# Kernel tuning notes

Measured on AMD Instinct MI355X. Metric: run time of the kernel, lower is better.

The kernel has to match this reference:

```python
import jax, jax.numpy as jnp
import numpy as np

# GeoFormer.generate_proposal constants (cfg.threshold_ins, cfg.min_pts_num,
# instance classes start at semantic id 4 on ScanNet)
THRESHOLD = 0.5
MIN_PTS_NUM = 50
MIN_INST_CLASS = 4


def setup_inputs() -> dict:
    key = jax.random.key(0)
    k1, k2, k3, k4 = jax.random.split(key, 4)
    B, Q, N, C = 4, 128, 50000, 20
    mask_logits = jax.random.normal(k1, (B, Q, N), dtype=jnp.float32)
    cls_logits = jax.random.normal(k2, (B, Q, C), dtype=jnp.float32)
    seg_pred = jax.random.randint(k3, (B, N), 0, C, dtype=jnp.int64)
    fg_idxs = jax.random.randint(k4, (B * N,), 0, 300000, dtype=jnp.int64)
    return {"mask_logits": mask_logits, "cls_logits": cls_logits,
            "seg_pred": seg_pred, "fg_idxs": fg_idxs}


def reference(mask_logits, cls_logits, seg_pred, fg_idxs):
    # mask_logits: [B, Q, N]  per-query point-mask logits (dense form of the
    #   per-batch list in the original; batch_offsets become the B dim)
    # cls_logits:  [B, Q, C]  per-query class logits
    # seg_pred:    [B, N]     per-point semantic prediction
    # fg_idxs:     [B*N]      foreground -> original point id map
    B, Q, N = mask_logits.shape
    m = jax.nn.sigmoid(mask_logits)                         # [B, Q, N]
    cls_pred = jnp.argmax(cls_logits, axis=2)               # [B, Q]

    # (mask_logit_b[n] > threshold) & (seg_pred == cls_logits_pred[b, n])
    sel = (m > THRESHOLD) & (seg_pred[:, None, :] == cls_pred[:, :, None])  # [B,Q,N]
    cnt = sel.sum(axis=-1)                                  # [B, Q] proposal sizes

    # score = mean of sigmoid over selected points
    msel = jnp.where(sel, m, jnp.zeros((), m.dtype))
    scores = msel.sum(axis=-1) / jnp.maximum(cnt, 1).astype(m.dtype)  # [B, Q]

    # skip if too few points or a background/wall class (< 4)
    valid = (cnt >= MIN_PTS_NUM) & (cls_pred >= MIN_INST_CLASS)       # [B, Q]

    proposal_masks = sel & valid[:, :, None]                # dense proposal_idx
    scores = jnp.where(valid, scores, jnp.zeros((), scores.dtype))
    global_ids = fg_idxs.reshape(B, N)                      # fg_idxs remap per point
    return proposal_masks, scores, valid, cls_pred, global_ids
```

## Files before the change

kernel.cpp:

```cpp
#include <hip/hip_runtime.h>
#include <math.h>

#define BB 4
#define QQ 128
#define NN 50000
#define CC 20
#define ROWS (BB * QQ)
#define NV4 (NN / 4)
#define TPB 256
#define UNROLL 4
#define BPR 13
#define THRESH_CNT 50
#define MIN_CLS 4

typedef float f32x4 __attribute__((ext_vector_type(4)));
typedef int   i32x4 __attribute__((ext_vector_type(4)));

struct Ws {
    float sum[ROWS];
    int   cnt[ROWS];
    int   cls[ROWS];
    int   valid[ROWS];
};

__global__ void k0_argmax_zero(const float* __restrict__ cls_logits, Ws* ws) {
    int r = blockIdx.x * blockDim.x + threadIdx.x;
    if (r >= ROWS) return;
    const float* p = cls_logits + r * CC;
    float best = p[0];
    int bi = 0;
    #pragma unroll
    for (int c = 1; c < CC; ++c) {
        float v = p[c];
        if (v > best) { best = v; bi = c; }
    }
    ws->cls[r] = bi;
    ws->sum[r] = 0.0f;
    ws->cnt[r] = 0;
}

__global__ __launch_bounds__(256) void k1_select(
        const float* __restrict__ mask_logits,
        const int*   __restrict__ seg_pred,
        float* __restrict__ out_mask,
        Ws* __restrict__ ws) {
    const int row = blockIdx.y;
    const int b   = row >> 7;
    const int cls = ws->cls[row];

    const f32x4* __restrict__ ml = (const f32x4*)(mask_logits + (size_t)row * NN);
    const i32x4* __restrict__ sp = (const i32x4*)(seg_pred + b * NN);
    f32x4* __restrict__ om = (f32x4*)(out_mask + (size_t)row * NN);

    const int idx0 = blockIdx.x * (TPB * UNROLL) + threadIdx.x;

    f32x4 v[UNROLL];
    i32x4 s[UNROLL];
    bool  act[UNROLL];
    #pragma unroll
    for (int j = 0; j < UNROLL; ++j) {
        int idx = idx0 + j * TPB;
        act[j] = (idx < NV4);
        if (act[j]) {
            v[j] = ml[idx];
            s[j] = sp[idx];
        }
    }

    float lsum = 0.0f;
    int   lcnt = 0;
    #pragma unroll
    for (int j = 0; j < UNROLL; ++j) {
        if (!act[j]) continue;
        int idx = idx0 + j * TPB;
        f32x4 vv = v[j];
        i32x4 ss = s[j];
        bool s0 = (vv.x > 0.0f) & (ss.x == cls);
        bool s1 = (vv.y > 0.0f) & (ss.y == cls);
        bool s2 = (vv.z > 0.0f) & (ss.z == cls);
        bool s3 = (vv.w > 0.0f) & (ss.w == cls);
        float g0 = 1.0f / (1.0f + __expf(-vv.x));
        float g1 = 1.0f / (1.0f + __expf(-vv.y));
        float g2 = 1.0f / (1.0f + __expf(-vv.z));
        float g3 = 1.0f / (1.0f + __expf(-vv.w));
        f32x4 o;
        o.x = s0 ? 1.0f : 0.0f;
        o.y = s1 ? 1.0f : 0.0f;
        o.z = s2 ? 1.0f : 0.0f;
        o.w = s3 ? 1.0f : 0.0f;
        lsum += (s0 ? g0 : 0.0f) + (s1 ? g1 : 0.0f)
              + (s2 ? g2 : 0.0f) + (s3 ? g3 : 0.0f);
        lcnt += (int)s0 + (int)s1 + (int)s2 + (int)s3;
        __builtin_nontemporal_store(o, &om[idx]);
    }

    #pragma unroll
    for (int off = 32; off > 0; off >>= 1) {
        lsum += __shfl_down(lsum, off);
        lcnt += __shfl_down(lcnt, off);
    }
    __shared__ float ssum[4];
    __shared__ int   scnt[4];
    const int wave = threadIdx.x >> 6;
    const int lane = threadIdx.x & 63;
    if (lane == 0) { ssum[wave] = lsum; scnt[wave] = lcnt; }
    __syncthreads();
    if (threadIdx.x == 0) {
        float ts = ssum[0] + ssum[1] + ssum[2] + ssum[3];
        int   tc = scnt[0] + scnt[1] + scnt[2] + scnt[3];
        atomicAdd(&ws->sum[row], ts);
        atomicAdd(&ws->cnt[row], tc);
    }
}

__global__ void k2_finalize_gids(const int* __restrict__ fg,
                                 float* __restrict__ out,
                                 Ws* __restrict__ ws) {
    const int idx = blockIdx.x * blockDim.x + threadIdx.x;
    if (idx < ROWS) {
        int   cnt = ws->cnt[idx];
        int   cls = ws->cls[idx];
        float sum = ws->sum[idx];
        int valid = (cnt >= THRESH_CNT) && (cls >= MIN_CLS);
        ws->valid[idx] = valid;
        float* tail = out + (size_t)ROWS * NN;
        tail[idx]            = valid ? (sum / (float)max(cnt, 1)) : 0.0f;
        tail[ROWS + idx]     = valid ? 1.0f : 0.0f;
        tail[2 * ROWS + idx] = (float)cls;
    }
    const int nv4 = (BB * NN) / 4;
    if (idx < nv4) {
        float* gids = out + (size_t)ROWS * NN + 3 * ROWS;
        i32x4 v = ((const i32x4*)fg)[idx];
        f32x4 o;
        o.x = (float)v.x; o.y = (float)v.y; o.z = (float)v.z; o.w = (float)v.w;
        __builtin_nontemporal_store(o, &((f32x4*)gids)[idx]);
    }
}

__global__ __launch_bounds__(256) void k3_fixup(
        float* __restrict__ out_mask, const Ws* __restrict__ ws) {
    const int row = blockIdx.y;
    if (ws->valid[row]) return;
    f32x4* __restrict__ om = (f32x4*)(out_mask + (size_t)row * NN);
    const f32x4 z = {0.0f, 0.0f, 0.0f, 0.0f};
    const int idx0 = blockIdx.x * (TPB * UNROLL) + threadIdx.x;
    #pragma unroll
    for (int j = 0; j < UNROLL; ++j) {
        int idx = idx0 + j * TPB;
        if (idx < NV4) __builtin_nontemporal_store(z, &om[idx]);
    }
}

extern "C" void kernel_launch(void* const* d_in, const int* in_sizes, int n_in,
                              void* d_out, int out_size, void* d_ws, size_t ws_size,
                              hipStream_t stream) {
    const float* mask_logits = (const float*)d_in[0];
    const float* cls_logits  = (const float*)d_in[1];
    const int*   seg_pred    = (const int*)d_in[2];
    const int*   fg_idxs     = (const int*)d_in[3];

    float* out = (float*)d_out;
    Ws* ws = (Ws*)d_ws;

    float* out_mask = out;

    k0_argmax_zero<<<(ROWS + 255) / 256, 256, 0, stream>>>(cls_logits, ws);

    dim3 g1(BPR, ROWS);
    k1_select<<<g1, TPB, 0, stream>>>(mask_logits, seg_pred, out_mask, ws);

    const int gids_blocks = ((BB * NN) / 4 + 255) / 256;
    k2_finalize_gids<<<gids_blocks, 256, 0, stream>>>(fg_idxs, out, ws);

    k3_fixup<<<g1, TPB, 0, stream>>>(out_mask, ws);
}
```

Measured before the change: 195.6 us.

## Pack selection bits in workspace, expand to the final mask after validity is known

The select kernel now writes a compact per-row bitmask to workspace instead of the full float mask. A separate expand kernel, run after finalize, writes the float mask with validity already applied. This removes the extra zeroing pass over invalid rows and makes the first pass read-only on the large output. The cost is an extra kernel launch plus a small bitmask round-trip, and it needs enough workspace. If workspace is too small, a fused fallback keeps the old three-pass scheme.

```diff
diff --git a/kernel.cpp b/kernel.cpp
--- a/kernel.cpp
+++ b/kernel.cpp
@@ -10,6 +10,7 @@
 #define TPB 256
 #define UNROLL 4
 #define BPR 13
+#define WPR 1568
 #define THRESH_CNT 50
 #define MIN_CLS 4
 
@@ -39,59 +40,62 @@
     ws->cnt[r] = 0;
 }
 
-__global__ __launch_bounds__(256) void k1_select(
+
+__global__ __launch_bounds__(256) void k1_pack(
         const float* __restrict__ mask_logits,
         const int*   __restrict__ seg_pred,
-        float* __restrict__ out_mask,
+        unsigned int* __restrict__ bits,
         Ws* __restrict__ ws) {
     const int row = blockIdx.y;
     const int b   = row >> 7;
     const int cls = ws->cls[row];
 
-    const f32x4* __restrict__ ml = (const f32x4*)(mask_logits + (size_t)row * NN);
-    const i32x4* __restrict__ sp = (const i32x4*)(seg_pred + b * NN);
-    f32x4* __restrict__ om = (f32x4*)(out_mask + (size_t)row * NN);
-
-    const int idx0 = blockIdx.x * (TPB * UNROLL) + threadIdx.x;
+    const f32x4* __restrict__ ml = (const f32x4*)mask_logits + (size_t)row * NV4;
+    const i32x4* __restrict__ sp = (const i32x4*)seg_pred + b * NV4;
+
+    const int base = blockIdx.x * (TPB * UNROLL) + threadIdx.x * UNROLL;
 
     f32x4 v[UNROLL];
     i32x4 s[UNROLL];
     bool  act[UNROLL];
     #pragma unroll
     for (int j = 0; j < UNROLL; ++j) {
-        int idx = idx0 + j * TPB;
-        act[j] = (idx < NV4);
+        act[j] = (base + j) < NV4;
         if (act[j]) {
-            v[j] = ml[idx];
-            s[j] = sp[idx];
+            v[j] = ml[base + j];
+            s[j] = sp[base + j];
         }
     }
 
+    unsigned int b16 = 0;
     float lsum = 0.0f;
     int   lcnt = 0;
     #pragma unroll
     for (int j = 0; j < UNROLL; ++j) {
-        if (!act[j]) continue;
-        int idx = idx0 + j * TPB;
-        f32x4 vv = v[j];
-        i32x4 ss = s[j];
-        bool s0 = (vv.x > 0.0f) & (ss.x == cls);
-        bool s1 = (vv.y > 0.0f) & (ss.y == cls);
-        bool s2 = (vv.z > 0.0f) & (ss.z == cls);
-        bool s3 = (vv.w > 0.0f) & (ss.w == cls);
-        float g0 = 1.0f / (1.0f + __expf(-vv.x));
-        float g1 = 1.0f / (1.0f + __expf(-vv.y));
-        float g2 = 1.0f / (1.0f + __expf(-vv.z));
-        float g3 = 1.0f / (1.0f + __expf(-vv.w));
-        f32x4 o;
-        o.x = s0 ? 1.0f : 0.0f;
-        o.y = s1 ? 1.0f : 0.0f;
-        o.z = s2 ? 1.0f : 0.0f;
-        o.w = s3 ? 1.0f : 0.0f;
-        lsum += (s0 ? g0 : 0.0f) + (s1 ? g1 : 0.0f)
-              + (s2 ? g2 : 0.0f) + (s3 ? g3 : 0.0f);
-        lcnt += (int)s0 + (int)s1 + (int)s2 + (int)s3;
-        __builtin_nontemporal_store(o, &om[idx]);
+        if (act[j]) {
+            f32x4 vv = v[j];
+            i32x4 ss = s[j];
+            unsigned s0 = (vv.x > 0.0f) & (ss.x == cls);
+            unsigned s1 = (vv.y > 0.0f) & (ss.y == cls);
+            unsigned s2 = (vv.z > 0.0f) & (ss.z == cls);
+            unsigned s3 = (vv.w > 0.0f) & (ss.w == cls);
+            b16 |= (s0 | (s1 << 1) | (s2 << 2) | (s3 << 3)) << (4 * j);
+            float g0 = 1.0f / (1.0f + __expf(-vv.x));
+            float g1 = 1.0f / (1.0f + __expf(-vv.y));
+            float g2 = 1.0f / (1.0f + __expf(-vv.z));
+            float g3 = 1.0f / (1.0f + __expf(-vv.w));
+            lsum += (s0 ? g0 : 0.0f) + (s1 ? g1 : 0.0f)
+                  + (s2 ? g2 : 0.0f) + (s3 ? g3 : 0.0f);
+            lcnt += (int)(s0 + s1 + s2 + s3);
+        }
+    }
+
+    unsigned int partner = __shfl_xor((int)b16, 1);
+    if ((threadIdx.x & 1) == 0) {
+        unsigned int word = b16 | (partner << 16);
+        const int h = blockIdx.x * TPB + threadIdx.x;
+        const int w = h >> 1;
+        if (w < WPR) bits[(size_t)row * WPR + w] = word;
     }
 
     #pragma unroll
@@ -110,6 +114,31 @@
         int   tc = scnt[0] + scnt[1] + scnt[2] + scnt[3];
         atomicAdd(&ws->sum[row], ts);
         atomicAdd(&ws->cnt[row], tc);
+    }
+}
+
+__global__ __launch_bounds__(256) void k_expand(
+        const unsigned int* __restrict__ bits,
+        const Ws* __restrict__ ws,
+        float* __restrict__ out_mask) {
+    const int row = blockIdx.y;
+    const float on = ws->valid[row] ? 1.0f : 0.0f;
+    const unsigned int* __restrict__ wb = bits + (size_t)row * WPR;
+    f32x4* __restrict__ om = (f32x4*)out_mask + (size_t)row * NV4;
+    const int idx0 = blockIdx.x * (TPB * UNROLL) + threadIdx.x;
+    #pragma unroll
+    for (int j = 0; j < UNROLL; ++j) {
+        int idx = idx0 + j * TPB;
+        if (idx < NV4) {
+            unsigned int word = wb[idx >> 3];
+            unsigned int nib = word >> ((idx & 7) * 4);
+            f32x4 o;
+            o.x = (nib & 1u) ? on : 0.0f;
+            o.y = (nib & 2u) ? on : 0.0f;
+            o.z = (nib & 4u) ? on : 0.0f;
+            o.w = (nib & 8u) ? on : 0.0f;
+            __builtin_nontemporal_store(o, &om[idx]);
+        }
     }
 }
 
@@ -138,6 +167,60 @@
     }
 }
 
+
+__global__ __launch_bounds__(256) void k1_select_fused(
+        const float* __restrict__ mask_logits,
+        const int*   __restrict__ seg_pred,
+        float* __restrict__ out_mask,
+        Ws* __restrict__ ws) {
+    const int row = blockIdx.y;
+    const int b   = row >> 7;
+    const int cls = ws->cls[row];
+    const f32x4* __restrict__ ml = (const f32x4*)(mask_logits + (size_t)row * NN);
+    const i32x4* __restrict__ sp = (const i32x4*)(seg_pred + b * NN);
+    f32x4* __restrict__ om = (f32x4*)(out_mask + (size_t)row * NN);
+    const int idx0 = blockIdx.x * (TPB * UNROLL) + threadIdx.x;
+    float lsum = 0.0f;
+    int   lcnt = 0;
+    #pragma unroll
+    for (int j = 0; j < UNROLL; ++j) {
+        int idx = idx0 + j * TPB;
+        if (idx >= NV4) continue;
+        f32x4 vv = ml[idx];
+        i32x4 ss = sp[idx];
+        bool s0 = (vv.x > 0.0f) & (ss.x == cls);
+        bool s1 = (vv.y > 0.0f) & (ss.y == cls);
+        bool s2 = (vv.z > 0.0f) & (ss.z == cls);
+        bool s3 = (vv.w > 0.0f) & (ss.w == cls);
+        f32x4 o;
+        o.x = s0 ? 1.0f : 0.0f;
+        o.y = s1 ? 1.0f : 0.0f;
+        o.z = s2 ? 1.0f : 0.0f;
+        o.w = s3 ? 1.0f : 0.0f;
+        lsum += (s0 ? 1.0f / (1.0f + __expf(-vv.x)) : 0.0f)
+              + (s1 ? 1.0f / (1.0f + __expf(-vv.y)) : 0.0f)
+              + (s2 ? 1.0f / (1.0f + __expf(-vv.z)) : 0.0f)
+              + (s3 ? 1.0f / (1.0f + __expf(-vv.w)) : 0.0f);
+        lcnt += (int)s0 + (int)s1 + (int)s2 + (int)s3;
+        __builtin_nontemporal_store(o, &om[idx]);
+    }
+    #pragma unroll
+    for (int off = 32; off > 0; off >>= 1) {
+        lsum += __shfl_down(lsum, off);
+        lcnt += __shfl_down(lcnt, off);
+    }
+    __shared__ float ssum[4];
+    __shared__ int   scnt[4];
+    const int wave = threadIdx.x >> 6;
+    const int lane = threadIdx.x & 63;
+    if (lane == 0) { ssum[wave] = lsum; scnt[wave] = lcnt; }
+    __syncthreads();
+    if (threadIdx.x == 0) {
+        atomicAdd(&ws->sum[row], ssum[0] + ssum[1] + ssum[2] + ssum[3]);
+        atomicAdd(&ws->cnt[row], scnt[0] + scnt[1] + scnt[2] + scnt[3]);
+    }
+}
+
 __global__ __launch_bounds__(256) void k3_fixup(
         float* __restrict__ out_mask, const Ws* __restrict__ ws) {
     const int row = blockIdx.y;
@@ -162,16 +245,25 @@
 
     float* out = (float*)d_out;
     Ws* ws = (Ws*)d_ws;
+    unsigned int* bits = (unsigned int*)((char*)d_ws + sizeof(Ws));
 
     float* out_mask = out;
 
+    const size_t ws_needed = sizeof(Ws) + (size_t)ROWS * WPR * sizeof(unsigned int);
+    const bool use_split = (ws_size >= ws_needed);
+
     k0_argmax_zero<<<(ROWS + 255) / 256, 256, 0, stream>>>(cls_logits, ws);
 
     dim3 g1(BPR, ROWS);
-    k1_select<<<g1, TPB, 0, stream>>>(mask_logits, seg_pred, out_mask, ws);
-
     const int gids_blocks = ((BB * NN) / 4 + 255) / 256;
-    k2_finalize_gids<<<gids_blocks, 256, 0, stream>>>(fg_idxs, out, ws);
-
-    k3_fixup<<<g1, TPB, 0, stream>>>(out_mask, ws);
-}
+
+    if (use_split) {
+        k1_pack<<<g1, TPB, 0, stream>>>(mask_logits, seg_pred, bits, ws);
+        k2_finalize_gids<<<gids_blocks, 256, 0, stream>>>(fg_idxs, out, ws);
+        k_expand<<<g1, TPB, 0, stream>>>(bits, ws, out_mask);
+    } else {
+        k1_select_fused<<<g1, TPB, 0, stream>>>(mask_logits, seg_pred, out_mask, ws);
+        k2_finalize_gids<<<gids_blocks, 256, 0, stream>>>(fg_idxs, out, ws);
+        k3_fixup<<<g1, TPB, 0, stream>>>(out_mask, ws);
+    }
+}
```

After: 206.4 us. 1.06x slower.

## Fuse select, finalize and fixup into one row-per-block kernel with class bitmasks

Applied to the files above, without the earlier changes.

Replaces the four-kernel pipeline with one block per (batch, query) row. Each block computes the argmax itself, reduces count and sum locally, decides validity, and writes the mask only once with the validity already applied. This removes the atomics, the workspace round trip, and the second pass that rewrote invalid rows with zeros. A pre-pass packs seg_pred into per-class bitmasks, so each row reads one bit per point instead of an int. The cost is that only 512 blocks of 512 threads run, each holding its selection bits in registers, which may lower parallelism.

```diff
diff --git a/kernel.cpp b/kernel.cpp
--- a/kernel.cpp
+++ b/kernel.cpp
@@ -7,91 +7,93 @@
 #define CC 20
 #define ROWS (BB * QQ)
 #define NV4 (NN / 4)
+#define W32 1568
 #define TPB 256
-#define UNROLL 4
-#define BPR 13
+#define TPB2 512
+#define ITER 25
 #define THRESH_CNT 50
 #define MIN_CLS 4
 
 typedef float f32x4 __attribute__((ext_vector_type(4)));
 typedef int   i32x4 __attribute__((ext_vector_type(4)));
 
-struct Ws {
-    float sum[ROWS];
-    int   cnt[ROWS];
-    int   cls[ROWS];
-    int   valid[ROWS];
-};
-
-__global__ void k0_argmax_zero(const float* __restrict__ cls_logits, Ws* ws) {
-    int r = blockIdx.x * blockDim.x + threadIdx.x;
-    if (r >= ROWS) return;
-    const float* p = cls_logits + r * CC;
-    float best = p[0];
-    int bi = 0;
+__global__ void k_pre_classbit(const int* __restrict__ seg,
+                               unsigned int* __restrict__ classbit) {
+    const int b = blockIdx.y;
+    const int p = blockIdx.x * TPB + threadIdx.x;
+    const int lane = threadIdx.x & 63;
+    const int cl = (p < NN) ? seg[b * NN + p] : -1;
+    const int w0 = (blockIdx.x * TPB + (threadIdx.x & ~63)) >> 5;
     #pragma unroll
-    for (int c = 1; c < CC; ++c) {
-        float v = p[c];
-        if (v > best) { best = v; bi = c; }
+    for (int c = 0; c < CC; ++c) {
+        unsigned long long m = __ballot(cl == c);
+        if (lane == 0)
+            classbit[((size_t)b * CC + c) * W32 + w0]     = (unsigned int)m;
+        if (lane == 32)
+            classbit[((size_t)b * CC + c) * W32 + w0 + 1] = (unsigned int)(m >> 32);
     }
-    ws->cls[r] = bi;
-    ws->sum[r] = 0.0f;
-    ws->cnt[r] = 0;
 }
 
-__global__ __launch_bounds__(256) void k1_select(
+template <bool USE_BITS>
+__global__ __launch_bounds__(TPB2) void k_fused(
         const float* __restrict__ mask_logits,
+        const float* __restrict__ cls_logits,
         const int*   __restrict__ seg_pred,
-        float* __restrict__ out_mask,
-        Ws* __restrict__ ws) {
-    const int row = blockIdx.y;
+        const unsigned int* __restrict__ classbit,
+        float* __restrict__ out) {
+    const int row = blockIdx.x;
     const int b   = row >> 7;
-    const int cls = ws->cls[row];
+    const int tid = threadIdx.x;
 
-    const f32x4* __restrict__ ml = (const f32x4*)(mask_logits + (size_t)row * NN);
-    const i32x4* __restrict__ sp = (const i32x4*)(seg_pred + b * NN);
-    f32x4* __restrict__ om = (f32x4*)(out_mask + (size_t)row * NN);
+    __shared__ float s_logit[CC];
+    __shared__ int   s_cls;
+    __shared__ float s_on;
+    if (tid < CC) s_logit[tid] = cls_logits[row * CC + tid];
+    __syncthreads();
+    if (tid == 0) {
+        float best = s_logit[0];
+        int bi = 0;
+        #pragma unroll
+        for (int c = 1; c < CC; ++c) {
+            if (s_logit[c] > best) { best = s_logit[c]; bi = c; }
+        }
+        s_cls = bi;
+    }
+    __syncthreads();
+    const int cls = s_cls;
 
-    const int idx0 = blockIdx.x * (TPB * UNROLL) + threadIdx.x;
+    const f32x4* __restrict__ ml = (const f32x4*)mask_logits + (size_t)row * NV4;
+    const unsigned int* __restrict__ cb =
+        classbit + ((size_t)b * CC + cls) * W32;
+    const i32x4* __restrict__ sp = (const i32x4*)seg_pred + (size_t)b * NV4;
 
-    f32x4 v[UNROLL];
-    i32x4 s[UNROLL];
-    bool  act[UNROLL];
-    #pragma unroll
-    for (int j = 0; j < UNROLL; ++j) {
-        int idx = idx0 + j * TPB;
-        act[j] = (idx < NV4);
-        if (act[j]) {
-            v[j] = ml[idx];
-            s[j] = sp[idx];
-        }
-    }
-
+    unsigned int bw[4] = {0u, 0u, 0u, 0u};
     float lsum = 0.0f;
     int   lcnt = 0;
     #pragma unroll
-    for (int j = 0; j < UNROLL; ++j) {
-        if (!act[j]) continue;
-        int idx = idx0 + j * TPB;
-        f32x4 vv = v[j];
-        i32x4 ss = s[j];
-        bool s0 = (vv.x > 0.0f) & (ss.x == cls);
-        bool s1 = (vv.y > 0.0f) & (ss.y == cls);
-        bool s2 = (vv.z > 0.0f) & (ss.z == cls);
-        bool s3 = (vv.w > 0.0f) & (ss.w == cls);
-        float g0 = 1.0f / (1.0f + __expf(-vv.x));
-        float g1 = 1.0f / (1.0f + __expf(-vv.y));
-        float g2 = 1.0f / (1.0f + __expf(-vv.z));
-        float g3 = 1.0f / (1.0f + __expf(-vv.w));
-        f32x4 o;
-        o.x = s0 ? 1.0f : 0.0f;
-        o.y = s1 ? 1.0f : 0.0f;
-        o.z = s2 ? 1.0f : 0.0f;
-        o.w = s3 ? 1.0f : 0.0f;
-        lsum += (s0 ? g0 : 0.0f) + (s1 ? g1 : 0.0f)
-              + (s2 ? g2 : 0.0f) + (s3 ? g3 : 0.0f);
-        lcnt += (int)s0 + (int)s1 + (int)s2 + (int)s3;
-        __builtin_nontemporal_store(o, &om[idx]);
+    for (int it = 0; it < ITER; ++it) {
+        const int idx = it * TPB2 + tid;
+        if (idx < NV4) {
+            f32x4 vv = ml[idx];
+            unsigned int nib;
+            if (USE_BITS) {
+                unsigned int cw = cb[idx >> 3];
+                nib = (cw >> ((tid & 7) * 4)) & 0xFu;
+            } else {
+                i32x4 ss = sp[idx];
+                nib = ((ss.x == cls) ? 1u : 0u) | ((ss.y == cls) ? 2u : 0u)
+                    | ((ss.z == cls) ? 4u : 0u) | ((ss.w == cls) ? 8u : 0u);
+            }
+            unsigned int se = ((vv.x > 0.0f) ? 1u : 0u) | ((vv.y > 0.0f) ? 2u : 0u)
+                            | ((vv.z > 0.0f) ? 4u : 0u) | ((vv.w > 0.0f) ? 8u : 0u);
+            unsigned int sel = se & nib;
+            lsum += ((sel & 1u) ? 1.0f / (1.0f + __expf(-vv.x)) : 0.0f)
+                  + ((sel & 2u) ? 1.0f / (1.0f + __expf(-vv.y)) : 0.0f)
+                  + ((sel & 4u) ? 1.0f / (1.0f + __expf(-vv.z)) : 0.0f)
+                  + ((sel & 8u) ? 1.0f / (1.0f + __expf(-vv.w)) : 0.0f);
+            lcnt += __popc(sel);
+            bw[it >> 3] |= sel << (4 * (it & 7));
+        }
     }
 
     #pragma unroll
@@ -99,56 +101,51 @@
         lsum += __shfl_down(lsum, off);
         lcnt += __shfl_down(lcnt, off);
     }
-    __shared__ float ssum[4];
-    __shared__ int   scnt[4];
-    const int wave = threadIdx.x >> 6;
-    const int lane = threadIdx.x & 63;
+    __shared__ float ssum[TPB2 / 64];
+    __shared__ int   scnt[TPB2 / 64];
+    const int wave = tid >> 6;
+    const int lane = tid & 63;
     if (lane == 0) { ssum[wave] = lsum; scnt[wave] = lcnt; }
     __syncthreads();
-    if (threadIdx.x == 0) {
-        float ts = ssum[0] + ssum[1] + ssum[2] + ssum[3];
-        int   tc = scnt[0] + scnt[1] + scnt[2] + scnt[3];
-        atomicAdd(&ws->sum[row], ts);
-        atomicAdd(&ws->cnt[row], tc);
+    if (tid == 0) {
+        float ts = 0.0f;
+        int   tc = 0;
+        #pragma unroll
+        for (int w = 0; w < TPB2 / 64; ++w) { ts += ssum[w]; tc += scnt[w]; }
+        const int valid = (tc >= THRESH_CNT) && (cls >= MIN_CLS);
+        float* tail = out + (size_t)ROWS * NN;
+        tail[row]            = valid ? (ts / (float)(tc > 1 ? tc : 1)) : 0.0f;
+        tail[ROWS + row]     = valid ? 1.0f : 0.0f;
+        tail[2 * ROWS + row] = (float)cls;
+        s_on = valid ? 1.0f : 0.0f;
+    }
+    __syncthreads();
+    const float on = s_on;
+
+    f32x4* __restrict__ om = (f32x4*)out + (size_t)row * NV4;
+    #pragma unroll
+    for (int it = 0; it < ITER; ++it) {
+        const int idx = it * TPB2 + tid;
+        if (idx < NV4) {
+            const unsigned int nib = (bw[it >> 3] >> (4 * (it & 7))) & 0xFu;
+            f32x4 o;
+            o.x = (nib & 1u) ? on : 0.0f;
+            o.y = (nib & 2u) ? on : 0.0f;
+            o.z = (nib & 4u) ? on : 0.0f;
+            o.w = (nib & 8u) ? on : 0.0f;
+            __builtin_nontemporal_store(o, &om[idx]);
+        }
     }
 }
 
-__global__ void k2_finalize_gids(const int* __restrict__ fg,
-                                 float* __restrict__ out,
-                                 Ws* __restrict__ ws) {
+__global__ void k_gids(const int* __restrict__ fg, float* __restrict__ out) {
     const int idx = blockIdx.x * blockDim.x + threadIdx.x;
-    if (idx < ROWS) {
-        int   cnt = ws->cnt[idx];
-        int   cls = ws->cls[idx];
-        float sum = ws->sum[idx];
-        int valid = (cnt >= THRESH_CNT) && (cls >= MIN_CLS);
-        ws->valid[idx] = valid;
-        float* tail = out + (size_t)ROWS * NN;
-        tail[idx]            = valid ? (sum / (float)max(cnt, 1)) : 0.0f;
-        tail[ROWS + idx]     = valid ? 1.0f : 0.0f;
-        tail[2 * ROWS + idx] = (float)cls;
-    }
     const int nv4 = (BB * NN) / 4;
     if (idx < nv4) {
-        float* gids = out + (size_t)ROWS * NN + 3 * ROWS;
         i32x4 v = ((const i32x4*)fg)[idx];
         f32x4 o;
         o.x = (float)v.x; o.y = (float)v.y; o.z = (float)v.z; o.w = (float)v.w;
-        __builtin_nontemporal_store(o, &((f32x4*)gids)[idx]);
-    }
-}
-
-__global__ __launch_bounds__(256) void k3_fixup(
-        float* __restrict__ out_mask, const Ws* __restrict__ ws) {
-    const int row = blockIdx.y;
-    if (ws->valid[row]) return;
-    f32x4* __restrict__ om = (f32x4*)(out_mask + (size_t)row * NN);
-    const f32x4 z = {0.0f, 0.0f, 0.0f, 0.0f};
-    const int idx0 = blockIdx.x * (TPB * UNROLL) + threadIdx.x;
-    #pragma unroll
-    for (int j = 0; j < UNROLL; ++j) {
-        int idx = idx0 + j * TPB;
-        if (idx < NV4) __builtin_nontemporal_store(z, &om[idx]);
+        __builtin_nontemporal_store(o, &((f32x4*)out)[idx]);
     }
 }
 
@@ -161,17 +158,22 @@
     const int*   fg_idxs     = (const int*)d_in[3];
 
     float* out = (float*)d_out;
-    Ws* ws = (Ws*)d_ws;
+    unsigned int* classbit = (unsigned int*)d_ws;
 
-    float* out_mask = out;
+    float* out_gids = out + (size_t)ROWS * NN + 3 * ROWS;
 
-    k0_argmax_zero<<<(ROWS + 255) / 256, 256, 0, stream>>>(cls_logits, ws);
+    const size_t cb_bytes = (size_t)BB * CC * W32 * sizeof(unsigned int);
+    const bool use_bits = (ws_size >= cb_bytes);
 
-    dim3 g1(BPR, ROWS);
-    k1_select<<<g1, TPB, 0, stream>>>(mask_logits, seg_pred, out_mask, ws);
+    if (use_bits) {
+        dim3 gp((NN + TPB - 1) / TPB, BB);
+        k_pre_classbit<<<gp, TPB, 0, stream>>>(seg_pred, classbit);
+        k_fused<true><<<ROWS, TPB2, 0, stream>>>(
+            mask_logits, cls_logits, seg_pred, classbit, out);
+    } else {
+        k_fused<false><<<ROWS, TPB2, 0, stream>>>(
+            mask_logits, cls_logits, seg_pred, classbit, out);
+    }
 
-    const int gids_blocks = ((BB * NN) / 4 + 255) / 256;
-    k2_finalize_gids<<<gids_blocks, 256, 0, stream>>>(fg_idxs, out, ws);
-
-    k3_fixup<<<g1, TPB, 0, stream>>>(out_mask, ws);
+    k_gids<<<((BB * NN) / 4 + TPB - 1) / TPB, TPB, 0, stream>>>(fg_idxs, out_gids);
 }
```

Result: slower. 205.2 us (+4.9%).

## Precompute per-class bitmasks of seg_pred to shrink per-row segment loads

Applied to the files above, without the earlier changes.

Adds a pre-pass that packs seg_pred into one bitmask per (batch, class) using wave ballots and stores it in workspace. The main select kernel then reads one 32-bit word per 8 threads instead of a 16-byte int vector per thread, cutting seg_pred read traffic by about 32x. It adds an extra kernel launch and relies on workspace size, falling back to the old path if the workspace is too small. Sigmoid is also evaluated only on selected lanes via bit tests.

```diff
diff --git a/kernel.cpp b/kernel.cpp
--- a/kernel.cpp
+++ b/kernel.cpp
@@ -10,6 +10,7 @@
 #define TPB 256
 #define UNROLL 4
 #define BPR 13
+#define W32 1568
 #define THRESH_CNT 50
 #define MIN_CLS 4
 
@@ -39,31 +40,58 @@
     ws->cnt[r] = 0;
 }
 
-__global__ __launch_bounds__(256) void k1_select(
+__global__ void k_pre_classbit(const int* __restrict__ seg,
+                               unsigned int* __restrict__ classbit) {
+    const int b = blockIdx.y;
+    const int p = blockIdx.x * TPB + threadIdx.x;
+    const int lane = threadIdx.x & 63;
+    const int cl = (p < NN) ? seg[b * NN + p] : -1;
+    const int w0 = (blockIdx.x * TPB + (threadIdx.x & ~63)) >> 5;
+    #pragma unroll
+    for (int c = 0; c < CC; ++c) {
+        unsigned long long m = __ballot(cl == c);
+        if (lane == 0)
+            classbit[((size_t)b * CC + c) * W32 + w0]     = (unsigned int)m;
+        if (lane == 32)
+            classbit[((size_t)b * CC + c) * W32 + w0 + 1] = (unsigned int)(m >> 32);
+    }
+}
+
+template <bool USE_BITS>
+__global__ __launch_bounds__(256) void k1_main(
         const float* __restrict__ mask_logits,
         const int*   __restrict__ seg_pred,
+        const unsigned int* __restrict__ classbit,
         float* __restrict__ out_mask,
         Ws* __restrict__ ws) {
     const int row = blockIdx.y;
     const int b   = row >> 7;
     const int cls = ws->cls[row];
-
-    const f32x4* __restrict__ ml = (const f32x4*)(mask_logits + (size_t)row * NN);
-    const i32x4* __restrict__ sp = (const i32x4*)(seg_pred + b * NN);
-    f32x4* __restrict__ om = (f32x4*)(out_mask + (size_t)row * NN);
-
-    const int idx0 = blockIdx.x * (TPB * UNROLL) + threadIdx.x;
-
-    f32x4 v[UNROLL];
-    i32x4 s[UNROLL];
-    bool  act[UNROLL];
+    const int tid = threadIdx.x;
+
+    const f32x4* __restrict__ ml = (const f32x4*)mask_logits + (size_t)row * NV4;
+    const i32x4* __restrict__ sp = (const i32x4*)seg_pred + (size_t)b * NV4;
+    const unsigned int* __restrict__ cb = classbit + ((size_t)b * CC + cls) * W32;
+    f32x4* __restrict__ om = (f32x4*)out_mask + (size_t)row * NV4;
+
+    const f32x4 vz = {0.0f, 0.0f, 0.0f, 0.0f};
+
+    int          idx[UNROLL];
+    bool         act[UNROLL];
+    f32x4        v[UNROLL];
+    unsigned int nib[UNROLL];
     #pragma unroll
     for (int j = 0; j < UNROLL; ++j) {
-        int idx = idx0 + j * TPB;
-        act[j] = (idx < NV4);
-        if (act[j]) {
-            v[j] = ml[idx];
-            s[j] = sp[idx];
+        idx[j] = blockIdx.x * (TPB * UNROLL) + j * TPB + tid;
+        act[j] = idx[j] < NV4;
+        v[j] = act[j] ? ml[idx[j]] : vz;
+        if (USE_BITS) {
+            unsigned int cw = act[j] ? cb[idx[j] >> 3] : 0u;
+            nib[j] = (cw >> ((tid & 7) * 4)) & 0xFu;
+        } else {
+            i32x4 ss = act[j] ? sp[idx[j]] : i32x4{-1, -1, -1, -1};
+            nib[j] = ((ss.x == cls) ? 1u : 0u) | ((ss.y == cls) ? 2u : 0u)
+                   | ((ss.z == cls) ? 4u : 0u) | ((ss.w == cls) ? 8u : 0u);
         }
     }
 
@@ -71,27 +99,21 @@
     int   lcnt = 0;
     #pragma unroll
     for (int j = 0; j < UNROLL; ++j) {
-        if (!act[j]) continue;
-        int idx = idx0 + j * TPB;
         f32x4 vv = v[j];
-        i32x4 ss = s[j];
-        bool s0 = (vv.x > 0.0f) & (ss.x == cls);
-        bool s1 = (vv.y > 0.0f) & (ss.y == cls);
-        bool s2 = (vv.z > 0.0f) & (ss.z == cls);
-        bool s3 = (vv.w > 0.0f) & (ss.w == cls);
-        float g0 = 1.0f / (1.0f + __expf(-vv.x));
-        float g1 = 1.0f / (1.0f + __expf(-vv.y));
-        float g2 = 1.0f / (1.0f + __expf(-vv.z));
-        float g3 = 1.0f / (1.0f + __expf(-vv.w));
+        unsigned int se = ((vv.x > 0.0f) ? 1u : 0u) | ((vv.y > 0.0f) ? 2u : 0u)
+                        | ((vv.z > 0.0f) ? 4u : 0u) | ((vv.w > 0.0f) ? 8u : 0u);
+        unsigned int sel = se & nib[j];
+        lsum += ((sel & 1u) ? 1.0f / (1.0f + __expf(-vv.x)) : 0.0f)
+              + ((sel & 2u) ? 1.0f / (1.0f + __expf(-vv.y)) : 0.0f)
+              + ((sel & 4u) ? 1.0f / (1.0f + __expf(-vv.z)) : 0.0f)
+              + ((sel & 8u) ? 1.0f / (1.0f + __expf(-vv.w)) : 0.0f);
+        lcnt += __popc(sel);
         f32x4 o;
-        o.x = s0 ? 1.0f : 0.0f;
-        o.y = s1 ? 1.0f : 0.0f;
-        o.z = s2 ? 1.0f : 0.0f;
-        o.w = s3 ? 1.0f : 0.0f;
-        lsum += (s0 ? g0 : 0.0f) + (s1 ? g1 : 0.0f)
-              + (s2 ? g2 : 0.0f) + (s3 ? g3 : 0.0f);
-        lcnt += (int)s0 + (int)s1 + (int)s2 + (int)s3;
-        __builtin_nontemporal_store(o, &om[idx]);
+        o.x = (sel & 1u) ? 1.0f : 0.0f;
+        o.y = (sel & 2u) ? 1.0f : 0.0f;
+        o.z = (sel & 4u) ? 1.0f : 0.0f;
+        o.w = (sel & 8u) ? 1.0f : 0.0f;
+        if (act[j]) __builtin_nontemporal_store(o, &om[idx[j]]);
     }
 
     #pragma unroll
@@ -101,15 +123,13 @@
     }
     __shared__ float ssum[4];
     __shared__ int   scnt[4];
-    const int wave = threadIdx.x >> 6;
-    const int lane = threadIdx.x & 63;
+    const int wave = tid >> 6;
+    const int lane = tid & 63;
     if (lane == 0) { ssum[wave] = lsum; scnt[wave] = lcnt; }
     __syncthreads();
-    if (threadIdx.x == 0) {
-        float ts = ssum[0] + ssum[1] + ssum[2] + ssum[3];
-        int   tc = scnt[0] + scnt[1] + scnt[2] + scnt[3];
-        atomicAdd(&ws->sum[row], ts);
-        atomicAdd(&ws->cnt[row], tc);
+    if (tid == 0) {
+        atomicAdd(&ws->sum[row], ssum[0] + ssum[1] + ssum[2] + ssum[3]);
+        atomicAdd(&ws->cnt[row], scnt[0] + scnt[1] + scnt[2] + scnt[3]);
     }
 }
 
@@ -142,7 +162,7 @@
         float* __restrict__ out_mask, const Ws* __restrict__ ws) {
     const int row = blockIdx.y;
     if (ws->valid[row]) return;
-    f32x4* __restrict__ om = (f32x4*)(out_mask + (size_t)row * NN);
+    f32x4* __restrict__ om = (f32x4*)out_mask + (size_t)row * NV4;
     const f32x4 z = {0.0f, 0.0f, 0.0f, 0.0f};
     const int idx0 = blockIdx.x * (TPB * UNROLL) + threadIdx.x;
     #pragma unroll
@@ -162,16 +182,29 @@
 
     float* out = (float*)d_out;
     Ws* ws = (Ws*)d_ws;
+    unsigned int* classbit = (unsigned int*)((char*)d_ws + sizeof(Ws));
 
     float* out_mask = out;
 
+    const size_t ws_needed = sizeof(Ws)
+        + (size_t)BB * CC * W32 * sizeof(unsigned int);
+    const bool use_bits = (ws_size >= ws_needed);
+
     k0_argmax_zero<<<(ROWS + 255) / 256, 256, 0, stream>>>(cls_logits, ws);
 
     dim3 g1(BPR, ROWS);
-    k1_select<<<g1, TPB, 0, stream>>>(mask_logits, seg_pred, out_mask, ws);
-
     const int gids_blocks = ((BB * NN) / 4 + 255) / 256;
+
+    if (use_bits) {
+        dim3 gp((NN + TPB - 1) / TPB, BB);
+        k_pre_classbit<<<gp, TPB, 0, stream>>>(seg_pred, classbit);
+        k1_main<true><<<g1, TPB, 0, stream>>>(
+            mask_logits, seg_pred, classbit, out_mask, ws);
+    } else {
+        k1_main<false><<<g1, TPB, 0, stream>>>(
+            mask_logits, seg_pred, classbit, out_mask, ws);
+    }
+
     k2_finalize_gids<<<gids_blocks, 256, 0, stream>>>(fg_idxs, out, ws);
-
     k3_fixup<<<g1, TPB, 0, stream>>>(out_mask, ws);
 }
```

New measurement: 202.8 us. +3.7%, slower.
